# Kernel optimization log

Hardware: AMD Instinct MI355X
Metric: run time of the kernel (lower is better)

The kernel has to match this reference:

```python
import jax, jax.numpy as jnp
import numpy as np

N, E = 30000, 480000
HID, NB, D = 256, 128, 2
SW = D * D * NB        # struct-encoder width = bundle_dim^2 * num_bundles = 512
NL, NSAGE = 2, 5       # outer BDL layers, SAGE layers inside struct encoder
OUT = 5
EPS = 1e-5


def _gelu(x):
    return jax.nn.gelu(x, approximate=False)  # torch nn.GELU default (exact)


def _mean_agg(x, src, dst):
    # mean over incoming edges: agg[v] = mean_{u->v} x[u]
    s = jax.ops.segment_sum(x[src], dst, num_segments=N)
    deg = jax.ops.segment_sum(jnp.ones((E,), x.dtype), dst, num_segments=N)
    return s / jnp.maximum(deg, 1.0)[:, None]


def _layernorm(x, g, b):
    m = jnp.mean(x, -1, keepdims=True)
    v = jnp.mean((x - m) ** 2, -1, keepdims=True)
    return (x - m) * jax.lax.rsqrt(v + EPS) * g + b


def _householder(X):
    # torch.nn.utils.parametrizations Orthogonal, orthogonal_map='householder':
    # Q = H_0 H_1 ... H_{d-1}, H_i = I - tau_i v_i v_i^T, v_i = strict-lower col i with unit diag
    d = X.shape[-1]
    A = jnp.tril(X, k=-1)
    tau = 2.0 / (1.0 + jnp.sum(A * A, axis=-2))  # [M, d]
    eye = jnp.eye(d, dtype=X.dtype)
    Q = jnp.broadcast_to(eye, X.shape)
    for i in range(d):
        v = A[:, :, i] + eye[i]
        Qv = jnp.einsum('mij,mj->mi', Q, v)
        Q = Q - tau[:, i, None, None] * Qv[:, :, None] * v[:, None, :]
    return Q


def _struct_encoder(h, src, dst, se_in_w, se_in_b, sage_w1, sage_b1, sage_w2, sage_b2, se_out_w, se_out_b):
    # Model('SAGE', 5, ...) with normalization='None'; dropout inactive in eval
    z = _gelu(h @ se_in_w + se_in_b)
    for i in range(NSAGE):
        m = _mean_agg(z, src, dst)
        zc = jnp.concatenate([z, m], axis=-1)  # SAGE: cat(self, mean(neigh))
        z = z + (_gelu(zc @ sage_w1[i] + sage_b1[i]) @ sage_w2[i] + sage_b2[i])
    return z @ se_out_w + se_out_b


def _forward(x, w_in, b_in, se_in_w, se_in_b, sage_w1, sage_b1, sage_w2, sage_b2,
             se_out_w, se_out_b, enc_w1, enc_b1, enc_w2, enc_b2, ln_g, ln_b,
             bdl_w1, bdl_b1, bdl_w2, bdl_b2, out_ln_g, out_ln_b, w_out, b_out, edge_index):
    src, dst = edge_index[0], edge_index[1]
    h = _gelu(x @ w_in + b_in)
    for k in range(NL):
        enc = _struct_encoder(h, src, dst, se_in_w, se_in_b, sage_w1, sage_b1,
                              sage_w2, sage_b2, se_out_w, se_out_b)
        nr = _gelu(enc @ enc_w1[k] + enc_b1[k]) @ enc_w2[k] + enc_b2[k]  # [N, SW]
        O = _householder(nr.reshape(N * NB, D, D)).reshape(N, NB, D, D)
        # BDL residual module: transport features through per-node bundle frames
        hn = _layernorm(h, ln_g[k], ln_b[k])
        hb = hn.reshape(N, NB, D)
        y = jnp.einsum('nbij,nbj->nbi', O, hb)                       # rotate into frame
        agg = _mean_agg(y.reshape(N, NB * D), src, dst).reshape(N, NB, D)
        msg = jnp.einsum('nbji,nbj->nbi', O, agg).reshape(N, NB * D)  # O^T transports back
        hc = jnp.concatenate([hn, msg], axis=-1)
        h = h + (_gelu(hc @ bdl_w1[k] + bdl_b1[k]) @ bdl_w2[k] + bdl_b2[k])
    h = _layernorm(h, out_ln_g, out_ln_b)
    return h @ w_out + b_out  # [N, OUT]; .squeeze(1) is a no-op for OUT>1


def _w(key, fan_in, shape):
    return jax.random.normal(key, shape, dtype=jnp.float32) / np.sqrt(fan_in)


def setup_inputs() -> dict:
    key = jax.random.key(0)
    ks = iter(jax.random.split(key, 40))
    f32 = jnp.float32
    return {
        'x': jax.random.normal(next(ks), (N, HID), dtype=f32),
        'edge_index': jax.random.randint(next(ks), (2, E), 0, N, dtype=jnp.int32),
        'w_in': _w(next(ks), HID, (HID, HID)), 'b_in': jnp.zeros((HID,), f32),
        'se_in_w': _w(next(ks), HID, (HID, SW)), 'se_in_b': jnp.zeros((SW,), f32),
        'sage_w1': _w(next(ks), 2 * SW, (NSAGE, 2 * SW, SW)), 'sage_b1': jnp.zeros((NSAGE, SW), f32),
        'sage_w2': _w(next(ks), SW, (NSAGE, SW, SW)), 'sage_b2': jnp.zeros((NSAGE, SW), f32),
        'se_out_w': _w(next(ks), SW, (SW, SW)), 'se_out_b': jnp.zeros((SW,), f32),
        'enc_w1': _w(next(ks), SW, (NL, SW, SW)), 'enc_b1': jnp.zeros((NL, SW), f32),
        'enc_w2': _w(next(ks), SW, (NL, SW, SW)), 'enc_b2': jnp.zeros((NL, SW), f32),
        'ln_g': jnp.ones((NL, HID), f32), 'ln_b': jnp.zeros((NL, HID), f32),
        'bdl_w1': _w(next(ks), 2 * HID, (NL, 2 * HID, HID)), 'bdl_b1': jnp.zeros((NL, HID), f32),
        'bdl_w2': _w(next(ks), HID, (NL, HID, HID)), 'bdl_b2': jnp.zeros((NL, HID), f32),
        'out_ln_g': jnp.ones((HID,), f32), 'out_ln_b': jnp.zeros((HID,), f32),
        'w_out': _w(next(ks), HID, (HID, OUT)), 'b_out': jnp.zeros((OUT,), f32),
    }


def reference(x, edge_index, w_in, b_in, se_in_w, se_in_b, sage_w1, sage_b1, sage_w2, sage_b2,
              se_out_w, se_out_b, enc_w1, enc_b1, enc_w2, enc_b2, ln_g, ln_b,
              bdl_w1, bdl_b1, bdl_w2, bdl_b2, out_ln_g, out_ln_b, w_out, b_out):
    return _forward(x, w_in, b_in, se_in_w, se_in_b, sage_w1, sage_b1, sage_w2, sage_b2,
                    se_out_w, se_out_b, enc_w1, enc_b1, enc_w2, enc_b2, ln_g, ln_b,
                    bdl_w1, bdl_b1, bdl_w2, bdl_b2, out_ln_g, out_ln_b, w_out, b_out, edge_index)
```

## Files before the change

### kernel.cpp

```cpp
#include <hip/hip_runtime.h>
#include <hip/hip_bf16.h>
#include <cstdint>
#include <cstddef>


typedef __attribute__((ext_vector_type(8))) short short8;
typedef __attribute__((ext_vector_type(4))) float f32x4;

__device__ __forceinline__ float gelu_exact(float x) {
  return 0.5f * x * (1.0f + erff(x * 0.7071067811865475f));
}
__device__ __forceinline__ unsigned short f2bf(float f) {
  __hip_bfloat16 b = __float2bfloat16(f);
  return *reinterpret_cast<unsigned short*>(&b);
}
__device__ __forceinline__ float bf2f(unsigned short u) {
  return __uint_as_float((unsigned)u << 16);
}
__device__ __forceinline__ float bflo(unsigned u) { return __uint_as_float(u << 16); }
__device__ __forceinline__ float bfhi(unsigned u) { return __uint_as_float(u & 0xffff0000u); }
__device__ __forceinline__ unsigned packbf(float f0, float f1) {
  return (unsigned)f2bf(f0) | ((unsigned)f2bf(f1) << 16);
}
__device__ __forceinline__ void gload16(const void* g, void* l) {
  __builtin_amdgcn_global_load_lds((const __attribute__((address_space(1))) void*)g,
                                   (__attribute__((address_space(3))) void*)l, 16, 0, 0);
}

__global__ void k_hist(const int* __restrict__ dst, int* __restrict__ deg, int E) {
  int i = blockIdx.x * 256 + threadIdx.x;
  if (i < E) atomicAdd(&deg[dst[i]], 1);
}

__global__ __launch_bounds__(1024)
void k_scan(const int* __restrict__ deg, int* __restrict__ rp, int* __restrict__ cur, int Nn) {
  __shared__ int part[1024];
  int t = threadIdx.x;
  int chunk = (Nn + 1023) >> 10;
  int s0 = t * chunk;
  int e0 = s0 + chunk; if (e0 > Nn) e0 = Nn;
  int s = 0;
  for (int i = s0; i < e0; ++i) s += deg[i];
  part[t] = s;
  __syncthreads();
  for (int off = 1; off < 1024; off <<= 1) {
    int v = (t >= off) ? part[t - off] : 0;
    __syncthreads();
    part[t] += v;
    __syncthreads();
  }
  int base = (t == 0) ? 0 : part[t - 1];
  for (int i = s0; i < e0; ++i) {
    rp[i] = base; cur[i] = base; base += deg[i];
  }
  if (t == 0) rp[Nn] = part[1023];
}

__global__ void k_fill(const int* __restrict__ src, const int* __restrict__ dst,
                       int* __restrict__ cur, int* __restrict__ srcs, int E) {
  int i = blockIdx.x * 256 + threadIdx.x;
  if (i < E) {
    int p = atomicAdd(&cur[dst[i]], 1);
    srcs[p] = src[i];
  }
}

__global__ void k_wT(const float* __restrict__ W, unsigned short* __restrict__ Wt, int K, int Nc) {
  const float* Ws = W + (size_t)blockIdx.y * K * Nc;
  unsigned short* Wd = Wt + (size_t)blockIdx.y * K * Nc;
  int idx = blockIdx.x * 256 + threadIdx.x;
  if (idx >= K * Nc) return;
  int k = idx % K, n = idx / K;
  Wd[(size_t)n * K + k] = f2bf(Ws[(size_t)k * Nc + n]);
}

__global__ void k_cast(const float* __restrict__ src, unsigned short* __restrict__ dst, int n) {
  int i = blockIdx.x * 256 + threadIdx.x;
  if (i < n) dst[i] = f2bf(src[i]);
}

template<int ACT, int RES, bool DUAL, bool W32, bool WBF>
__global__ __launch_bounds__(256)
void k_mfma(const unsigned short* __restrict__ A1, const unsigned short* __restrict__ A2,
            int K1, int K2,
            const unsigned short* __restrict__ Wt, const float* __restrict__ bias,
            const float* R32, const unsigned short* Rbf,
            float* C32, unsigned short* Cbf, int M, int Nc) {
  const int mb_cnt = (M + 127) >> 7;
  const int nb_cnt = Nc >> 7;
  int u = blockIdx.x;
  int xcd = u & 7;
  int rest = u >> 3;
  int nb = rest % nb_cnt;
  int mb = (rest / nb_cnt) * 8 + xcd;
  if (mb >= mb_cnt) return;
  const int m0 = mb << 7, n0 = nb << 7;

  __shared__ unsigned short As[128 * 64];
  __shared__ unsigned short Bs[128 * 64];
  const int tid = threadIdx.x;
  const int lane = tid & 63, wv = tid >> 6;
  const int wr = (wv >> 1) * 64, wc = (wv & 1) * 64;
  const int rA = lane & 15, kg = lane >> 4;
  const int Ktot = K1 + K2;

  f32x4 acc[4][4];
#pragma unroll
  for (int m = 0; m < 4; ++m)
#pragma unroll
    for (int n = 0; n < 4; ++n)
#pragma unroll
      for (int r = 0; r < 4; ++r) acc[m][n][r] = 0.f;

  for (int k0 = 0; k0 < Ktot; k0 += 64) {
    const unsigned short* Asrc; int kc, lda;
    if (!DUAL || k0 < K1) { Asrc = A1; kc = k0; lda = K1; }
    else                  { Asrc = A2; kc = k0 - K1; lda = K2; }
    __syncthreads();
#pragma unroll
    for (int is = 0; is < 4; ++is) {
      int chunk = is * 256 + tid;
      int row = chunk >> 3, seg = chunk & 7;
      int ks = seg ^ (row & 7);
      int gm = m0 + row; gm = gm < M ? gm : M - 1;
      gload16(Asrc + (size_t)gm * lda + kc + ks * 8,
              (char*)As + (size_t)(is * 256 + (wv << 6)) * 16);
      gload16(Wt + (size_t)(n0 + row) * Ktot + k0 + ks * 8,
              (char*)Bs + (size_t)(is * 256 + (wv << 6)) * 16);
    }
    __syncthreads();
#pragma unroll
    for (int kk = 0; kk < 2; ++kk) {
      short8 af[4], bfr[4];
#pragma unroll
      for (int m = 0; m < 4; ++m) {
        int row = wr + m * 16 + rA;
        int ks = (kk * 4 + kg) ^ (row & 7);
        af[m] = *reinterpret_cast<const short8*>((const char*)As + row * 128 + ks * 16);
      }
#pragma unroll
      for (int n = 0; n < 4; ++n) {
        int col = wc + n * 16 + rA;
        int ks = (kk * 4 + kg) ^ (col & 7);
        bfr[n] = *reinterpret_cast<const short8*>((const char*)Bs + col * 128 + ks * 16);
      }
#pragma unroll
      for (int m = 0; m < 4; ++m)
#pragma unroll
        for (int n = 0; n < 4; ++n)
          acc[m][n] = __builtin_amdgcn_mfma_f32_16x16x32_bf16(af[m], bfr[n], acc[m][n], 0, 0, 0);
    }
  }

#pragma unroll
  for (int m = 0; m < 4; ++m) {
    int gr0 = m0 + wr + m * 16 + kg * 4;
#pragma unroll
    for (int n = 0; n < 4; ++n) {
      int gc = n0 + wc + n * 16 + rA;
      float bv = bias[gc];
#pragma unroll
      for (int r = 0; r < 4; ++r) {
        int gr = gr0 + r;
        if (gr < M) {
          float v = acc[m][n][r] + bv;
          if (ACT == 1) v = gelu_exact(v);
          if (RES == 1) v += R32[(size_t)gr * Nc + gc];
          if (RES == 2) v += bf2f(Rbf[(size_t)gr * Nc + gc]);
          if (W32) C32[(size_t)gr * Nc + gc] = v;
          if (WBF) Cbf[(size_t)gr * Nc + gc] = f2bf(v);
        }
      }
    }
  }
}

template<int W, bool ROT>
__global__ __launch_bounds__(256)
void k_agg(const unsigned short* __restrict__ X, const int* __restrict__ rp,
           const int* __restrict__ srcs, const float* __restrict__ o,
           unsigned short* __restrict__ out, int Nn) {
  int wid = (blockIdx.x * 256 + threadIdx.x) >> 6;
  int lane = threadIdx.x & 63;
  if (wid >= Nn) return;
  constexpr int PE = W / 64;
  float a[PE];
#pragma unroll
  for (int p = 0; p < PE; ++p) a[p] = 0.f;
  int beg = rp[wid], end = rp[wid + 1];
  for (int e = beg; e < end; ++e) {
    int s = srcs[e];
    const unsigned* row = reinterpret_cast<const unsigned*>(X + (size_t)s * W) + lane * (PE / 2);
    if (PE == 8) {
      uint4 v = *reinterpret_cast<const uint4*>(row);
      a[0] += bflo(v.x); a[1] += bfhi(v.x); a[2] += bflo(v.y); a[3] += bfhi(v.y);
      a[4] += bflo(v.z); a[5] += bfhi(v.z); a[6] += bflo(v.w); a[7] += bfhi(v.w);
    } else {
      uint2 v = *reinterpret_cast<const uint2*>(row);
      a[0] += bflo(v.x); a[1] += bfhi(v.x); a[2] += bflo(v.y); a[3] += bfhi(v.y);
    }
  }
  float inv = (end > beg) ? 1.0f / (float)(end - beg) : 0.0f;
#pragma unroll
  for (int p = 0; p < PE; ++p) a[p] *= inv;
  if (ROT) {
    float4 oc = *reinterpret_cast<const float4*>(o + (size_t)wid * 256 + lane * 4);
    float m0 = oc.x * a[0] - oc.y * a[1];
    float m1 = oc.y * a[0] + oc.x * a[1];
    float m2 = oc.z * a[2] - oc.w * a[3];
    float m3 = oc.w * a[2] + oc.z * a[3];
    a[0] = m0; a[1] = m1; a[2] = m2; a[3] = m3;
  }
  unsigned short* op = out + (size_t)wid * W + lane * PE;
  if (PE == 8) {
    uint4 rv;
    rv.x = packbf(a[0], a[1]); rv.y = packbf(a[2], a[3]);
    rv.z = packbf(a[4], a[5]); rv.w = packbf(a[6], a[7]);
    *reinterpret_cast<uint4*>(op) = rv;
  } else {
    uint2 rv;
    rv.x = packbf(a[0], a[1]); rv.y = packbf(a[2], a[3]);
    *reinterpret_cast<uint2*>(op) = rv;
  }
}

__global__ void k_oparams(const unsigned short* __restrict__ nr, float* __restrict__ o, int total) {
  int idx = blockIdx.x * 256 + threadIdx.x;
  if (idx >= total) return;
  float x = bf2f(nr[(size_t)idx * 4 + 2]);
  float inv = 1.0f / (1.0f + x * x);
  o[(size_t)idx * 2]     = (x * x - 1.0f) * inv;
  o[(size_t)idx * 2 + 1] = 2.0f * x * inv;
}

__global__ __launch_bounds__(256)
void k_ln_rot(const float* __restrict__ h, const float* __restrict__ o,
              const float* __restrict__ g, const float* __restrict__ b,
              unsigned short* __restrict__ hn, unsigned short* __restrict__ y, int Nn) {
  int wid = (blockIdx.x * 256 + threadIdx.x) >> 6;
  int lane = threadIdx.x & 63;
  if (wid >= Nn) return;
  float4 v = reinterpret_cast<const float4*>(h + (size_t)wid * 256)[lane];
  float s = v.x + v.y + v.z + v.w;
  float ss = v.x * v.x + v.y * v.y + v.z * v.z + v.w * v.w;
#pragma unroll
  for (int off = 1; off < 64; off <<= 1) { s += __shfl_xor(s, off); ss += __shfl_xor(ss, off); }
  float mean = s * (1.0f / 256.0f);
  float var = ss * (1.0f / 256.0f) - mean * mean;
  float rs = rsqrtf(var + 1e-5f);
  float4 gg = reinterpret_cast<const float4*>(g)[lane];
  float4 bb = reinterpret_cast<const float4*>(b)[lane];
  float h0 = (v.x - mean) * rs * gg.x + bb.x;
  float h1 = (v.y - mean) * rs * gg.y + bb.y;
  float h2 = (v.z - mean) * rs * gg.z + bb.z;
  float h3 = (v.w - mean) * rs * gg.w + bb.w;
  uint2 hv; hv.x = packbf(h0, h1); hv.y = packbf(h2, h3);
  *reinterpret_cast<uint2*>(hn + (size_t)wid * 256 + lane * 4) = hv;
  float4 oc = *reinterpret_cast<const float4*>(o + (size_t)wid * 256 + lane * 4);
  float y0 =  oc.x * h0 + oc.y * h1;
  float y1 = -oc.y * h0 + oc.x * h1;
  float y2 =  oc.z * h2 + oc.w * h3;
  float y3 = -oc.w * h2 + oc.z * h3;
  uint2 yv; yv.x = packbf(y0, y1); yv.y = packbf(y2, y3);
  *reinterpret_cast<uint2*>(y + (size_t)wid * 256 + lane * 4) = yv;
}

__global__ __launch_bounds__(256)
void k_final(const float* __restrict__ h, const float* __restrict__ g,
             const float* __restrict__ b, const float* __restrict__ wout,
             const float* __restrict__ bout, float* __restrict__ out, int Nn) {
  int wid = (blockIdx.x * 256 + threadIdx.x) >> 6;
  int lane = threadIdx.x & 63;
  if (wid >= Nn) return;
  float4 v = reinterpret_cast<const float4*>(h + (size_t)wid * 256)[lane];
  float s = v.x + v.y + v.z + v.w;
  float ss = v.x * v.x + v.y * v.y + v.z * v.z + v.w * v.w;
#pragma unroll
  for (int off = 1; off < 64; off <<= 1) { s += __shfl_xor(s, off); ss += __shfl_xor(ss, off); }
  float mean = s * (1.0f / 256.0f);
  float var = ss * (1.0f / 256.0f) - mean * mean;
  float rs = rsqrtf(var + 1e-5f);
  float4 gg = reinterpret_cast<const float4*>(g)[lane];
  float4 bb = reinterpret_cast<const float4*>(b)[lane];
  float hv[4];
  hv[0] = (v.x - mean) * rs * gg.x + bb.x;
  hv[1] = (v.y - mean) * rs * gg.y + bb.y;
  hv[2] = (v.z - mean) * rs * gg.z + bb.z;
  hv[3] = (v.w - mean) * rs * gg.w + bb.w;
  int c0 = lane * 4;
  float dots[5];
#pragma unroll
  for (int j = 0; j < 5; ++j) {
    float p = hv[0] * wout[(size_t)(c0 + 0) * 5 + j] + hv[1] * wout[(size_t)(c0 + 1) * 5 + j]
            + hv[2] * wout[(size_t)(c0 + 2) * 5 + j] + hv[3] * wout[(size_t)(c0 + 3) * 5 + j];
#pragma unroll
    for (int off = 1; off < 64; off <<= 1) p += __shfl_xor(p, off);
    dots[j] = p;
  }
  if (lane == 0) {
#pragma unroll
    for (int j = 0; j < 5; ++j) out[(size_t)wid * 5 + j] = dots[j] + bout[j];
  }
}

extern "C" void kernel_launch(void* const* d_in, const int* in_sizes, int n_in,
                              void* d_out, int out_size, void* d_ws, size_t ws_size,
                              hipStream_t stream) {
  const float* x       = (const float*)d_in[0];
  const int*   ei      = (const int*)  d_in[1];
  const float* w_in    = (const float*)d_in[2];
  const float* b_in    = (const float*)d_in[3];
  const float* se_in_w = (const float*)d_in[4];
  const float* se_in_b = (const float*)d_in[5];
  const float* sage_w1 = (const float*)d_in[6];
  const float* sage_b1 = (const float*)d_in[7];
  const float* sage_w2 = (const float*)d_in[8];
  const float* sage_b2 = (const float*)d_in[9];
  const float* se_out_w= (const float*)d_in[10];
  const float* se_out_b= (const float*)d_in[11];
  const float* enc_w1  = (const float*)d_in[12];
  const float* enc_b1  = (const float*)d_in[13];
  const float* enc_w2  = (const float*)d_in[14];
  const float* enc_b2  = (const float*)d_in[15];
  const float* ln_g    = (const float*)d_in[16];
  const float* ln_b    = (const float*)d_in[17];
  const float* bdl_w1  = (const float*)d_in[18];
  const float* bdl_b1  = (const float*)d_in[19];
  const float* bdl_w2  = (const float*)d_in[20];
  const float* bdl_b2  = (const float*)d_in[21];
  const float* oln_g   = (const float*)d_in[22];
  const float* oln_b   = (const float*)d_in[23];
  const float* w_out   = (const float*)d_in[24];
  const float* b_out   = (const float*)d_in[25];
  float* out = (float*)d_out;

  const int HID = 256, SW = 512;
  const int N = in_sizes[0] / HID;
  const int E = in_sizes[1] / 2;

  float* ws = (float*)d_ws;
  float* h32 = ws;
  float* o   = h32 + (size_t)N * HID;
  unsigned short* h_bf = (unsigned short*)(o + (size_t)N * HID);
  unsigned short* z_bf = h_bf + (size_t)N * HID;
  unsigned short* t_bf = z_bf + (size_t)N * SW;
  unsigned short* u_bf = t_bf + (size_t)N * SW;
  unsigned short* wts = u_bf + (size_t)N * SW;
  size_t off = 0;
  unsigned short* wt_in    = wts + off; off += 256 * 256;
  unsigned short* wt_se_in = wts + off; off += 512 * 256;
  unsigned short* wt_sage1 = wts + off; off += (size_t)5 * 512 * 1024;
  unsigned short* wt_sage2 = wts + off; off += (size_t)5 * 512 * 512;
  unsigned short* wt_se_out= wts + off; off += 512 * 512;
  unsigned short* wt_enc1  = wts + off; off += (size_t)2 * 512 * 512;
  unsigned short* wt_enc2  = wts + off; off += (size_t)2 * 512 * 512;
  unsigned short* wt_bdl1  = wts + off; off += (size_t)2 * 256 * 512;
  unsigned short* wt_bdl2  = wts + off; off += (size_t)2 * 256 * 256;
  int* deg  = (int*)(wts + off);
  int* rp   = deg + N;
  int* cur  = rp + N + 1;
  int* srcs = cur + N;
  size_t need = (size_t)((char*)(srcs + E) - (char*)d_ws);
  if (ws_size < need) return;

  unsigned short* xbf = u_bf;
  unsigned short* hn  = z_bf;
  unsigned short* y   = z_bf + (size_t)N * HID;
  unsigned short* msg = t_bf;
  unsigned short* g2  = u_bf;

  const int* esrc = ei;
  const int* edst = ei + E;

  auto cdiv = [](int a, int b) { return (a + b - 1) / b; };
  dim3 blk(256);
  int mb_cnt = cdiv(N, 128);
  int mgrp = cdiv(mb_cnt, 8);
  int g_g256 = mgrp * 8 * 2;
  int g_g512 = mgrp * 8 * 4;
  int gw = cdiv(N * 64, 256);

  hipMemsetAsync(deg, 0, sizeof(int) * N, stream);
  k_hist<<<cdiv(E, 256), blk, 0, stream>>>(edst, deg, E);
  k_scan<<<1, 1024, 0, stream>>>(deg, rp, cur, N);
  k_fill<<<cdiv(E, 256), blk, 0, stream>>>(esrc, edst, cur, srcs, E);

  auto wT = [&](const float* W, unsigned short* Wt, int K, int Nc, int cnt) {
    k_wT<<<dim3(cdiv(K * Nc, 256), cnt), blk, 0, stream>>>(W, Wt, K, Nc);
  };
  wT(w_in, wt_in, 256, 256, 1);
  wT(se_in_w, wt_se_in, 256, 512, 1);
  wT(sage_w1, wt_sage1, 1024, 512, 5);
  wT(sage_w2, wt_sage2, 512, 512, 5);
  wT(se_out_w, wt_se_out, 512, 512, 1);
  wT(enc_w1, wt_enc1, 512, 512, 2);
  wT(enc_w2, wt_enc2, 512, 512, 2);
  wT(bdl_w1, wt_bdl1, 512, 256, 2);
  wT(bdl_w2, wt_bdl2, 256, 256, 2);
  k_cast<<<cdiv(N * HID, 256), blk, 0, stream>>>(x, xbf, N * HID);

  k_mfma<1, 0, false, true, true><<<g_g256, blk, 0, stream>>>(
      xbf, nullptr, 256, 0, wt_in, b_in, nullptr, nullptr, h32, h_bf, N, 256);

  for (int k = 0; k < 2; ++k) {
    k_mfma<1, 0, false, false, true><<<g_g512, blk, 0, stream>>>(
        h_bf, nullptr, 256, 0, wt_se_in, se_in_b, nullptr, nullptr, nullptr, z_bf, N, 512);
    for (int i = 0; i < 5; ++i) {
      k_agg<512, false><<<gw, blk, 0, stream>>>(z_bf, rp, srcs, nullptr, t_bf, N);
      k_mfma<1, 0, true, false, true><<<g_g512, blk, 0, stream>>>(
          z_bf, t_bf, 512, 512, wt_sage1 + (size_t)i * 512 * 1024,
          sage_b1 + (size_t)i * SW, nullptr, nullptr, nullptr, u_bf, N, 512);
      k_mfma<0, 2, false, false, true><<<g_g512, blk, 0, stream>>>(
          u_bf, nullptr, 512, 0, wt_sage2 + (size_t)i * 512 * 512,
          sage_b2 + (size_t)i * SW, nullptr, z_bf, nullptr, z_bf, N, 512);
    }
    k_mfma<0, 0, false, false, true><<<g_g512, blk, 0, stream>>>(
        z_bf, nullptr, 512, 0, wt_se_out, se_out_b, nullptr, nullptr, nullptr, t_bf, N, 512);
    k_mfma<1, 0, false, false, true><<<g_g512, blk, 0, stream>>>(
        t_bf, nullptr, 512, 0, wt_enc1 + (size_t)k * 512 * 512,
        enc_b1 + (size_t)k * SW, nullptr, nullptr, nullptr, u_bf, N, 512);
    k_mfma<0, 0, false, false, true><<<g_g512, blk, 0, stream>>>(
        u_bf, nullptr, 512, 0, wt_enc2 + (size_t)k * 512 * 512,
        enc_b2 + (size_t)k * SW, nullptr, nullptr, nullptr, t_bf, N, 512);
    k_oparams<<<cdiv(N * 128, 256), blk, 0, stream>>>(t_bf, o, N * 128);
    k_ln_rot<<<gw, blk, 0, stream>>>(h32, o, ln_g + (size_t)k * HID, ln_b + (size_t)k * HID, hn, y, N);
    k_agg<256, true><<<gw, blk, 0, stream>>>(y, rp, srcs, o, msg, N);
    k_mfma<1, 0, true, false, true><<<g_g256, blk, 0, stream>>>(
        hn, msg, 256, 256, wt_bdl1 + (size_t)k * 256 * 512,
        bdl_b1 + (size_t)k * HID, nullptr, nullptr, nullptr, g2, N, 256);
    k_mfma<0, 1, false, true, true><<<g_g256, blk, 0, stream>>>(
        g2, nullptr, 256, 0, wt_bdl2 + (size_t)k * 256 * 256,
        bdl_b2 + (size_t)k * HID, h32, nullptr, h32, h_bf, N, 256);
  }

  k_final<<<gw, blk, 0, stream>>>(h32, oln_g, oln_b, w_out, b_out, out, N);
}
```

Baseline: 2.696 ms.

## Split mean-aggregation into column slices with persistent grid-stride blocks

Replaces the one-wave-per-node aggregation, where each lane loads a 16-byte chunk of the full row, with a column-sliced kernel. Consecutive blocks handle different 64-column slices of the same node group, so each lane reads a single bf16 element per edge. Blocks grid-stride over node groups, the edge loop is unrolled by four, and edge indices and outputs use nontemporal loads and stores. The intent is better L2 locality for gathered rows across slices and more memory-level parallelism, at the cost of narrow 2-byte accesses, and the index arrays are now re-read once per slice.

Result: slower. 3.655 ms (+35.6%).

```diff
diff --git a/kernel.cpp b/kernel.cpp
--- a/kernel.cpp
+++ b/kernel.cpp
@@ -175,52 +175,49 @@
   }
 }
 
-template<int W, bool ROT>
+template<int W, int LSL, bool ROT>
 __global__ __launch_bounds__(256)
-void k_agg(const unsigned short* __restrict__ X, const int* __restrict__ rp,
-           const int* __restrict__ srcs, const float* __restrict__ o,
-           unsigned short* __restrict__ out, int Nn) {
-  int wid = (blockIdx.x * 256 + threadIdx.x) >> 6;
-  int lane = threadIdx.x & 63;
-  if (wid >= Nn) return;
-  constexpr int PE = W / 64;
-  float a[PE];
-#pragma unroll
-  for (int p = 0; p < PE; ++p) a[p] = 0.f;
-  int beg = rp[wid], end = rp[wid + 1];
-  for (int e = beg; e < end; ++e) {
-    int s = srcs[e];
-    const unsigned* row = reinterpret_cast<const unsigned*>(X + (size_t)s * W) + lane * (PE / 2);
-    if (PE == 8) {
-      uint4 v = *reinterpret_cast<const uint4*>(row);
-      a[0] += bflo(v.x); a[1] += bfhi(v.x); a[2] += bflo(v.y); a[3] += bfhi(v.y);
-      a[4] += bflo(v.z); a[5] += bfhi(v.z); a[6] += bflo(v.w); a[7] += bfhi(v.w);
-    } else {
-      uint2 v = *reinterpret_cast<const uint2*>(row);
-      a[0] += bflo(v.x); a[1] += bfhi(v.x); a[2] += bflo(v.y); a[3] += bfhi(v.y);
-    }
-  }
-  float inv = (end > beg) ? 1.0f / (float)(end - beg) : 0.0f;
-#pragma unroll
-  for (int p = 0; p < PE; ++p) a[p] *= inv;
-  if (ROT) {
-    float4 oc = *reinterpret_cast<const float4*>(o + (size_t)wid * 256 + lane * 4);
-    float m0 = oc.x * a[0] - oc.y * a[1];
-    float m1 = oc.y * a[0] + oc.x * a[1];
-    float m2 = oc.z * a[2] - oc.w * a[3];
-    float m3 = oc.w * a[2] + oc.z * a[3];
-    a[0] = m0; a[1] = m1; a[2] = m2; a[3] = m3;
-  }
-  unsigned short* op = out + (size_t)wid * W + lane * PE;
-  if (PE == 8) {
-    uint4 rv;
-    rv.x = packbf(a[0], a[1]); rv.y = packbf(a[2], a[3]);
-    rv.z = packbf(a[4], a[5]); rv.w = packbf(a[6], a[7]);
-    *reinterpret_cast<uint4*>(op) = rv;
-  } else {
-    uint2 rv;
-    rv.x = packbf(a[0], a[1]); rv.y = packbf(a[2], a[3]);
-    *reinterpret_cast<uint2*>(op) = rv;
+void k_aggs(const unsigned short* __restrict__ X, const int* __restrict__ rp,
+            const int* __restrict__ srcs, const float* __restrict__ o,
+            unsigned short* __restrict__ out, int Nn) {
+  constexpr int SL = 1 << LSL;
+  static_assert(W / SL == 64, "64 columns per slice");
+  const int u = blockIdx.x;
+  const int sl = u & (SL - 1);
+  const int g = u >> LSL;
+  const int ngrp = (int)(gridDim.x >> LSL);
+  const int wv = threadIdx.x >> 6, lane = threadIdx.x & 63;
+  const int c = sl * 64 + lane;
+  const int stride = ngrp * 4;
+
+  for (int v = g * 4 + wv; v < Nn; v += stride) {
+    int beg = __builtin_nontemporal_load(rp + v);
+    int end = __builtin_nontemporal_load(rp + v + 1);
+    float a = 0.f;
+    int e = beg;
+    for (; e + 4 <= end; e += 4) {
+      int s0 = __builtin_nontemporal_load(srcs + e);
+      int s1 = __builtin_nontemporal_load(srcs + e + 1);
+      int s2 = __builtin_nontemporal_load(srcs + e + 2);
+      int s3 = __builtin_nontemporal_load(srcs + e + 3);
+      float v0 = bf2f(X[(size_t)s0 * W + c]);
+      float v1 = bf2f(X[(size_t)s1 * W + c]);
+      float v2 = bf2f(X[(size_t)s2 * W + c]);
+      float v3 = bf2f(X[(size_t)s3 * W + c]);
+      a += (v0 + v1) + (v2 + v3);
+    }
+    for (; e < end; ++e) {
+      int s0 = __builtin_nontemporal_load(srcs + e);
+      a += bf2f(X[(size_t)s0 * W + c]);
+    }
+    float inv = (end > beg) ? 1.0f / (float)(end - beg) : 0.0f;
+    a *= inv;
+    if (ROT) {
+      float ap = __shfl_xor(a, 1);
+      float2 cs = *reinterpret_cast<const float2*>(o + (size_t)v * 256 + (c & ~1));
+      a = (lane & 1) ? (cs.y * ap + cs.x * a) : (cs.x * a - cs.y * ap);
+    }
+    __builtin_nontemporal_store(f2bf(a), out + (size_t)v * W + c);
   }
 }
 
@@ -379,6 +376,8 @@
   int g_g256 = mgrp * 8 * 2;
   int g_g512 = mgrp * 8 * 4;
   int gw = cdiv(N * 64, 256);
+  int g_agg512 = 8 * 940;
+  int g_agg256 = 4 * 940;
 
   hipMemsetAsync(deg, 0, sizeof(int) * N, stream);
   k_hist<<<cdiv(E, 256), blk, 0, stream>>>(edst, deg, E);
@@ -406,7 +405,7 @@
     k_mfma<1, 0, false, false, true><<<g_g512, blk, 0, stream>>>(
         h_bf, nullptr, 256, 0, wt_se_in, se_in_b, nullptr, nullptr, nullptr, z_bf, N, 512);
     for (int i = 0; i < 5; ++i) {
-      k_agg<512, false><<<gw, blk, 0, stream>>>(z_bf, rp, srcs, nullptr, t_bf, N);
+      k_aggs<512, 3, false><<<g_agg512, blk, 0, stream>>>(z_bf, rp, srcs, nullptr, t_bf, N);
       k_mfma<1, 0, true, false, true><<<g_g512, blk, 0, stream>>>(
           z_bf, t_bf, 512, 512, wt_sage1 + (size_t)i * 512 * 1024,
           sage_b1 + (size_t)i * SW, nullptr, nullptr, nullptr, u_bf, N, 512);
@@ -424,7 +423,7 @@
         enc_b2 + (size_t)k * SW, nullptr, nullptr, nullptr, t_bf, N, 512);
     k_oparams<<<cdiv(N * 128, 256), blk, 0, stream>>>(t_bf, o, N * 128);
     k_ln_rot<<<gw, blk, 0, stream>>>(h32, o, ln_g + (size_t)k * HID, ln_b + (size_t)k * HID, hn, y, N);
-    k_agg<256, true><<<gw, blk, 0, stream>>>(y, rp, srcs, o, msg, N);
+    k_aggs<256, 2, true><<<g_agg256, blk, 0, stream>>>(y, rp, srcs, o, msg, N);
     k_mfma<1, 0, true, false, true><<<g_g256, blk, 0, stream>>>(
         hn, msg, 256, 256, wt_bdl1 + (size_t)k * 256 * 512,
         bdl_b1 + (size_t)k * HID, nullptr, nullptr, nullptr, g2, N, 256);
```

## Double-buffer GEMM LDS tiles and fuse rotation-parameter computation into epilogue

Applied to the files above, without the earlier changes.

The MFMA GEMM kernel now stages A/B tiles into two LDS buffers and prefetches tile t+2 while computing tile t. It uses explicit vmcnt waits, barriers and a raised wave priority around the MFMA block, so global-to-LDS loads overlap with matrix math instead of serialising. Separately, the enc_w2 GEMM now computes the rotation cos/sin parameters directly in its epilogue. This removes the k_oparams kernel and the bf16 write and read of that intermediate. The cost is double the LDS per block, which may lower occupancy, plus hand-written waitcnt logic that depends on a fixed count of outstanding loads.

New measurement: 2.610 ms. 1.03x faster.

```diff
diff --git a/kernel.cpp b/kernel.cpp
--- a/kernel.cpp
+++ b/kernel.cpp
@@ -26,6 +26,7 @@
   __builtin_amdgcn_global_load_lds((const __attribute__((address_space(1))) void*)g,
                                    (__attribute__((address_space(3))) void*)l, 16, 0, 0);
 }
+#define SCHEDB() __builtin_amdgcn_sched_barrier(0)
 
 __global__ void k_hist(const int* __restrict__ dst, int* __restrict__ deg, int E) {
   int i = blockIdx.x * 256 + threadIdx.x;
@@ -79,13 +80,13 @@
   if (i < n) dst[i] = f2bf(src[i]);
 }
 
-template<int ACT, int RES, bool DUAL, bool W32, bool WBF>
+template<int ACT, int RES, bool DUAL, bool W32, bool WBF, bool OP>
 __global__ __launch_bounds__(256)
 void k_mfma(const unsigned short* __restrict__ A1, const unsigned short* __restrict__ A2,
             int K1, int K2,
             const unsigned short* __restrict__ Wt, const float* __restrict__ bias,
             const float* R32, const unsigned short* Rbf,
-            float* C32, unsigned short* Cbf, int M, int Nc) {
+            float* C32, unsigned short* Cbf, float* Op, int M, int Nc) {
   const int mb_cnt = (M + 127) >> 7;
   const int nb_cnt = Nc >> 7;
   int u = blockIdx.x;
@@ -96,13 +97,14 @@
   if (mb >= mb_cnt) return;
   const int m0 = mb << 7, n0 = nb << 7;
 
-  __shared__ unsigned short As[128 * 64];
-  __shared__ unsigned short Bs[128 * 64];
+  __shared__ unsigned short As[2][128 * 64];
+  __shared__ unsigned short Bs[2][128 * 64];
   const int tid = threadIdx.x;
   const int lane = tid & 63, wv = tid >> 6;
   const int wr = (wv >> 1) * 64, wc = (wv & 1) * 64;
   const int rA = lane & 15, kg = lane >> 4;
   const int Ktot = K1 + K2;
+  const int nt = Ktot >> 6;
 
   f32x4 acc[4][4];
 #pragma unroll
@@ -112,44 +114,65 @@
 #pragma unroll
       for (int r = 0; r < 4; ++r) acc[m][n][r] = 0.f;
 
-  for (int k0 = 0; k0 < Ktot; k0 += 64) {
+  auto stage = [&](int t, int b) {
+    int k0 = t << 6;
     const unsigned short* Asrc; int kc, lda;
     if (!DUAL || k0 < K1) { Asrc = A1; kc = k0; lda = K1; }
     else                  { Asrc = A2; kc = k0 - K1; lda = K2; }
-    __syncthreads();
 #pragma unroll
     for (int is = 0; is < 4; ++is) {
       int chunk = is * 256 + tid;
       int row = chunk >> 3, seg = chunk & 7;
       int ks = seg ^ (row & 7);
       int gm = m0 + row; gm = gm < M ? gm : M - 1;
-      gload16(Asrc + (size_t)gm * lda + kc + ks * 8,
-              (char*)As + (size_t)(is * 256 + (wv << 6)) * 16);
-      gload16(Wt + (size_t)(n0 + row) * Ktot + k0 + ks * 8,
-              (char*)Bs + (size_t)(is * 256 + (wv << 6)) * 16);
+      gload16(Asrc + (size_t)gm * lda + kc + ks * 8, (char*)As[b] + (size_t)chunk * 16);
+      gload16(Wt + (size_t)(n0 + row) * Ktot + k0 + ks * 8, (char*)Bs[b] + (size_t)chunk * 16);
     }
-    __syncthreads();
+  };
+
+  stage(0, 0);
+  if (nt > 1) stage(1, 1);
+
+  for (int t = 0; t < nt; ++t) {
+    const int b = t & 1;
+    if (t + 1 < nt) asm volatile("s_waitcnt vmcnt(8)" ::: "memory");
+    else            asm volatile("s_waitcnt vmcnt(0)" ::: "memory");
+    SCHEDB();
+    __builtin_amdgcn_s_barrier();
+    SCHEDB();
+
+    short8 af[2][4], bq[2][4];
 #pragma unroll
     for (int kk = 0; kk < 2; ++kk) {
-      short8 af[4], bfr[4];
 #pragma unroll
       for (int m = 0; m < 4; ++m) {
         int row = wr + m * 16 + rA;
         int ks = (kk * 4 + kg) ^ (row & 7);
-        af[m] = *reinterpret_cast<const short8*>((const char*)As + row * 128 + ks * 16);
+        af[kk][m] = *reinterpret_cast<const short8*>((const char*)As[b] + row * 128 + ks * 16);
       }
 #pragma unroll
       for (int n = 0; n < 4; ++n) {
         int col = wc + n * 16 + rA;
         int ks = (kk * 4 + kg) ^ (col & 7);
-        bfr[n] = *reinterpret_cast<const short8*>((const char*)Bs + col * 128 + ks * 16);
+        bq[kk][n] = *reinterpret_cast<const short8*>((const char*)Bs[b] + col * 128 + ks * 16);
       }
+    }
+    asm volatile("s_waitcnt lgkmcnt(0)" ::: "memory");
+    SCHEDB();
+    __builtin_amdgcn_s_barrier();
+    SCHEDB();
+    if (t + 2 < nt) stage(t + 2, b);
+
+    __builtin_amdgcn_s_setprio(1);
+#pragma unroll
+    for (int kk = 0; kk < 2; ++kk)
 #pragma unroll
       for (int m = 0; m < 4; ++m)
 #pragma unroll
         for (int n = 0; n < 4; ++n)
-          acc[m][n] = __builtin_amdgcn_mfma_f32_16x16x32_bf16(af[m], bfr[n], acc[m][n], 0, 0, 0);
-    }
+          acc[m][n] = __builtin_amdgcn_mfma_f32_16x16x32_bf16(af[kk][m], bq[kk][n],
+                                                              acc[m][n], 0, 0, 0);
+    __builtin_amdgcn_s_setprio(0);
   }
 
 #pragma unroll
@@ -169,6 +192,14 @@
           if (RES == 2) v += bf2f(Rbf[(size_t)gr * Nc + gc]);
           if (W32) C32[(size_t)gr * Nc + gc] = v;
           if (WBF) Cbf[(size_t)gr * Nc + gc] = f2bf(v);
+          if (OP) {
+            if ((rA & 3) == 2) {
+              float iv = 1.0f / (1.0f + v * v);
+              float* op = Op + (size_t)gr * 256 + ((gc >> 2) << 1);
+              op[0] = (v * v - 1.0f) * iv;
+              op[1] = 2.0f * v * iv;
+            }
+          }
         }
       }
     }
@@ -222,15 +253,6 @@
     rv.x = packbf(a[0], a[1]); rv.y = packbf(a[2], a[3]);
     *reinterpret_cast<uint2*>(op) = rv;
   }
-}
-
-__global__ void k_oparams(const unsigned short* __restrict__ nr, float* __restrict__ o, int total) {
-  int idx = blockIdx.x * 256 + threadIdx.x;
-  if (idx >= total) return;
-  float x = bf2f(nr[(size_t)idx * 4 + 2]);
-  float inv = 1.0f / (1.0f + x * x);
-  o[(size_t)idx * 2]     = (x * x - 1.0f) * inv;
-  o[(size_t)idx * 2 + 1] = 2.0f * x * inv;
 }
 
 __global__ __launch_bounds__(256)
@@ -399,38 +421,37 @@
   wT(bdl_w2, wt_bdl2, 256, 256, 2);
   k_cast<<<cdiv(N * HID, 256), blk, 0, stream>>>(x, xbf, N * HID);
 
-  k_mfma<1, 0, false, true, true><<<g_g256, blk, 0, stream>>>(
-      xbf, nullptr, 256, 0, wt_in, b_in, nullptr, nullptr, h32, h_bf, N, 256);
+  k_mfma<1, 0, false, true, true, false><<<g_g256, blk, 0, stream>>>(
+      xbf, nullptr, 256, 0, wt_in, b_in, nullptr, nullptr, h32, h_bf, nullptr, N, 256);
 
   for (int k = 0; k < 2; ++k) {
-    k_mfma<1, 0, false, false, true><<<g_g512, blk, 0, stream>>>(
-        h_bf, nullptr, 256, 0, wt_se_in, se_in_b, nullptr, nullptr, nullptr, z_bf, N, 512);
+    k_mfma<1, 0, false, false, true, false><<<g_g512, blk, 0, stream>>>(
+        h_bf, nullptr, 256, 0, wt_se_in, se_in_b, nullptr, nullptr, nullptr, z_bf, nullptr, N, 512);
     for (int i = 0; i < 5; ++i) {
       k_agg<512, false><<<gw, blk, 0, stream>>>(z_bf, rp, srcs, nullptr, t_bf, N);
-      k_mfma<1, 0, true, false, true><<<g_g512, blk, 0, stream>>>(
+      k_mfma<1, 0, true, false, true, false><<<g_g512, blk, 0, stream>>>(
           z_bf, t_bf, 512, 512, wt_sage1 + (size_t)i * 512 * 1024,
-          sage_b1 + (size_t)i * SW, nullptr, nullptr, nullptr, u_bf, N, 512);
-      k_mfma<0, 2, false, false, true><<<g_g512, blk, 0, stream>>>(
+          sage_b1 + (size_t)i * SW, nullptr, nullptr, nullptr, u_bf, nullptr, N, 512);
+      k_mfma<0, 2, false, false, true, false><<<g_g512, blk, 0, stream>>>(
           u_bf, nullptr, 512, 0, wt_sage2 + (size_t)i * 512 * 512,
-          sage_b2 + (size_t)i * SW, nullptr, z_bf, nullptr, z_bf, N, 512);
+          sage_b2 + (size_t)i * SW, nullptr, z_bf, nullptr, z_bf, nullptr, N, 512);
     }
-    k_mfma<0, 0, false, false, true><<<g_g512, blk, 0, stream>>>(
-        z_bf, nullptr, 512, 0, wt_se_out, se_out_b, nullptr, nullptr, nullptr, t_bf, N, 512);
-    k_mfma<1, 0, false, false, true><<<g_g512, blk, 0, stream>>>(
+    k_mfma<0, 0, false, false, true, false><<<g_g512, blk, 0, stream>>>(
+        z_bf, nullptr, 512, 0, wt_se_out, se_out_b, nullptr, nullptr, nullptr, t_bf, nullptr, N, 512);
+    k_mfma<1, 0, false, false, true, false><<<g_g512, blk, 0, stream>>>(
         t_bf, nullptr, 512, 0, wt_enc1 + (size_t)k * 512 * 512,
-        enc_b1 + (size_t)k * SW, nullptr, nullptr, nullptr, u_bf, N, 512);
-    k_mfma<0, 0, false, false, true><<<g_g512, blk, 0, stream>>>(
+        enc_b1 + (size_t)k * SW, nullptr, nullptr, nullptr, u_bf, nullptr, N, 512);
+    k_mfma<0, 0, false, false, false, true><<<g_g512, blk, 0, stream>>>(
         u_bf, nullptr, 512, 0, wt_enc2 + (size_t)k * 512 * 512,
-        enc_b2 + (size_t)k * SW, nullptr, nullptr, nullptr, t_bf, N, 512);
-    k_oparams<<<cdiv(N * 128, 256), blk, 0, stream>>>(t_bf, o, N * 128);
+        enc_b2 + (size_t)k * SW, nullptr, nullptr, nullptr, nullptr, o, N, 512);
     k_ln_rot<<<gw, blk, 0, stream>>>(h32, o, ln_g + (size_t)k * HID, ln_b + (size_t)k * HID, hn, y, N);
     k_agg<256, true><<<gw, blk, 0, stream>>>(y, rp, srcs, o, msg, N);
-    k_mfma<1, 0, true, false, true><<<g_g256, blk, 0, stream>>>(
+    k_mfma<1, 0, true, false, true, false><<<g_g256, blk, 0, stream>>>(
         hn, msg, 256, 256, wt_bdl1 + (size_t)k * 256 * 512,
-        bdl_b1 + (size_t)k * HID, nullptr, nullptr, nullptr, g2, N, 256);
-    k_mfma<0, 1, false, true, true><<<g_g256, blk, 0, stream>>>(
+        bdl_b1 + (size_t)k * HID, nullptr, nullptr, nullptr, g2, nullptr, N, 256);
+    k_mfma<0, 1, false, true, true, false><<<g_g256, blk, 0, stream>>>(
         g2, nullptr, 256, 0, wt_bdl2 + (size_t)k * 256 * 256,
-        bdl_b2 + (size_t)k * HID, h32, nullptr, h32, h_bf, N, 256);
+        bdl_b2 + (size_t)k * HID, h32, nullptr, h32, h_bf, nullptr, N, 256);
   }
 
   k_final<<<gw, blk, 0, stream>>>(h32, oln_g, oln_b, w_out, b_out, out, N);
```
